# Performance work log

Measured on AMD Instinct MI355X. Metric: run time of the kernel, lower is better.

## Reference

```python
import jax, jax.numpy as jnp
import numpy as np

HQ, HKV, HD = 8, 4, 256          # query heads, kv heads, head dim
SW = 1024                         # sliding window (layer_idx=0 is even -> window active)
EPS = 1e-6
SCALE = 256.0 ** -0.5             # query_pre_attn_scalar ** -0.5
THETA = 10000.0
NEG = jnp.finfo(jnp.float32).min


def _rms_norm(x, w):
    # Gemma2 RMSNorm: fp32 variance, weight applied as (1 + kernel)
    var = jnp.mean(jnp.square(x.astype(jnp.float32)), axis=-1, keepdims=True)
    xn = x / jnp.sqrt(var + EPS)
    return (1.0 + w) * xn


def _rope(q, k, positions):
    # standard rotate-half RoPE over full head_dim
    inv = 1.0 / (THETA ** (jnp.arange(0, HD, 2, dtype=jnp.float32) / HD))  # [HD/2]
    freqs = positions.astype(jnp.float32)[..., None] * inv                  # [B,S,HD/2]
    emb = jnp.concatenate([freqs, freqs], axis=-1)                          # [B,S,HD]
    cos = jnp.cos(emb)[:, :, None, :]
    sin = jnp.sin(emb)[:, :, None, :]
    def rot(x):
        return jnp.concatenate([-x[..., HD // 2:], x[..., :HD // 2]], axis=-1)
    return q * cos + rot(q) * sin, k * cos + rot(k) * sin


def setup_inputs() -> dict:
    key = jax.random.key(0)
    ks = jax.random.split(key, 12)
    B, S, D, I = 1, 2048, 2304, 9216
    std = 0.02
    return {
        "hidden_states": jax.random.normal(ks[0], (B, S, D), jnp.float32),
        "attention_mask": jnp.ones((B, S), jnp.int32),
        "position_ids": jnp.broadcast_to(jnp.arange(S, dtype=jnp.int32)[None], (B, S)),
        "wq": jax.random.normal(ks[1], (D, HQ * HD), jnp.float32) * std,
        "wk": jax.random.normal(ks[2], (D, HKV * HD), jnp.float32) * std,
        "wv": jax.random.normal(ks[3], (D, HKV * HD), jnp.float32) * std,
        "wo": jax.random.normal(ks[4], (HQ * HD, D), jnp.float32) * std,
        "w_gate": jax.random.normal(ks[5], (D, I), jnp.float32) * std,
        "w_up": jax.random.normal(ks[6], (D, I), jnp.float32) * std,
        "w_down": jax.random.normal(ks[7], (I, D), jnp.float32) * std,
        "ln_in": jax.random.uniform(ks[8], (D,), jnp.float32) * 0.1,
        "ln_post_attn": jax.random.uniform(ks[9], (D,), jnp.float32) * 0.1,
        "ln_pre_ffn": jax.random.uniform(ks[10], (D,), jnp.float32) * 0.1,
        "ln_post_ffn": jax.random.uniform(ks[11], (D,), jnp.float32) * 0.1,
    }


def _attention(h, attention_mask, position_ids, wq, wk, wv, wo):
    B, S, _ = h.shape
    q = (h @ wq).reshape(B, S, HQ, HD)
    k = (h @ wk).reshape(B, S, HKV, HD)
    v = (h @ wv).reshape(B, S, HKV, HD)
    q, k = _rope(q, k, position_ids)
    # GQA: repeat kv heads
    groups = HQ // HKV
    k = jnp.repeat(k, groups, axis=2)  # [B,S,HQ,HD]
    v = jnp.repeat(v, groups, axis=2)
    # combined mask: causal AND within sliding window AND padding mask
    i = jnp.arange(S)[:, None]
    j = jnp.arange(S)[None, :]
    keep = (j <= i) & ((i - j) < SW)                       # [S,S]
    keep = keep[None, None] & (attention_mask[:, None, None, :] > 0)  # [B,1,S,S]
    bias = jnp.where(keep, 0.0, NEG).astype(jnp.float32)
    scores = jnp.einsum("bqhd,bkhd->bhqk", q, k) * SCALE + bias
    probs = jax.nn.softmax(scores, axis=-1)
    out = jnp.einsum("bhqk,bkhd->bqhd", probs, v).reshape(B, S, HQ * HD)
    return out @ wo


def reference(hidden_states, attention_mask, position_ids, wq, wk, wv, wo,
              w_gate, w_up, w_down, ln_in, ln_post_attn, ln_pre_ffn, ln_post_ffn):
    # Gemma2 decoder layer with sandwich norms
    residual = hidden_states
    h = _rms_norm(hidden_states, ln_in)
    attn = _attention(h, attention_mask, position_ids, wq, wk, wv, wo)
    h = _rms_norm(attn, ln_post_attn)
    x = residual + h
    residual = x
    h = _rms_norm(x, ln_pre_ffn)
    h = (jax.nn.gelu(h @ w_gate, approximate=True) * (h @ w_up)) @ w_down
    h = _rms_norm(h, ln_post_ffn)
    return residual + h
```

## Files before the change

kernel.cpp:

```cpp
#include <hip/hip_runtime.h>
#include <stdint.h>

typedef unsigned short u16;
typedef unsigned int u32;
typedef __bf16 bf16x8 __attribute__((ext_vector_type(8)));
typedef float f32x4 __attribute__((ext_vector_type(4)));

#define S_LEN 2048
#define DMODEL 2304
#define DFF 9216
#define NHQ 8
#define NHKV 4
#define HDIM 256
#define SWIN 1024

__device__ __forceinline__ u16 f2bf(float f) {
  u32 u = __float_as_uint(f);
  u = (u + 0x7FFFu + ((u >> 16) & 1)) >> 16;
  return (u16)u;
}
__device__ __forceinline__ float bf2f(u16 h) {
  return __uint_as_float(((u32)h) << 16);
}

__device__ __forceinline__ void gload_lds16(const void* g, void* l) {
  __builtin_amdgcn_global_load_lds((const __attribute__((address_space(1))) u32*)g,
                                   (__attribute__((address_space(3))) u32*)l, 16, 0, 0);
}

template <int N>
__device__ __forceinline__ void wait_vmcnt() {
  if constexpr (N == 0) asm volatile("s_waitcnt vmcnt(0)" ::: "memory");
  else if constexpr (N == 4) asm volatile("s_waitcnt vmcnt(4)" ::: "memory");
  else if constexpr (N == 5) asm volatile("s_waitcnt vmcnt(5)" ::: "memory");
  else if constexpr (N == 6) asm volatile("s_waitcnt vmcnt(6)" ::: "memory");
  else if constexpr (N == 8) asm volatile("s_waitcnt vmcnt(8)" ::: "memory");
}

__device__ __forceinline__ float gelu_t(float x) {
  float u = 0.7978845608f * (x + 0.044715f * x * x * x);
  float e = __expf(2.f * u);
  float t = 1.f - 2.f / (e + 1.f);
  return 0.5f * x * (1.f + t);
}

__global__ __launch_bounds__(256) void transpose_convert(
    const float* __restrict__ in, u16* __restrict__ out, int K, int N, int stride) {
  __shared__ float t[32][130];
  const int k0 = blockIdx.x * 32, n0 = blockIdx.y * 128;
  const int tx = threadIdx.x & 31, ty = threadIdx.x >> 5;
#pragma unroll
  for (int r = 0; r < 4; ++r) {
    const float4 v = *(const float4*)&in[(size_t)(k0 + ty + r * 8) * stride + n0 + 4 * tx];
    t[ty + r * 8][4 * tx + 0] = v.x;
    t[ty + r * 8][4 * tx + 1] = v.y;
    t[ty + r * 8][4 * tx + 2] = v.z;
    t[ty + r * 8][4 * tx + 3] = v.w;
  }
  __syncthreads();
  const int kk = threadIdx.x & 15, nn = threadIdx.x >> 4;
#pragma unroll
  for (int r = 0; r < 8; ++r) {
    const int n = nn + r * 16;
    const u32 p = (u32)f2bf(t[2 * kk][n]) | ((u32)f2bf(t[2 * kk + 1][n]) << 16);
    *(u32*)&out[(size_t)(n0 + n) * K + k0 + 2 * kk] = p;
  }
}

__global__ __launch_bounds__(256) void vpack_kernel(
    const float* __restrict__ qkvf, u16* __restrict__ vtile) {
  __shared__ float t[32][33];
  const int s0 = blockIdx.x * 32, d0 = blockIdx.y * 32, kvh = blockIdx.z;
  const int tx = threadIdx.x & 31, ty = threadIdx.x >> 5;
#pragma unroll
  for (int r = 0; r < 4; ++r)
    t[ty + r * 8][tx] = qkvf[(size_t)(s0 + ty + r * 8) * 4096 + 3072 + kvh * HDIM + d0 + tx];
  __syncthreads();
  const int kk = threadIdx.x & 15, nn = threadIdx.x >> 4;
#pragma unroll
  for (int r = 0; r < 2; ++r) {
    const int d = nn + r * 16;
    const u32 p = (u32)f2bf(t[2 * kk][d]) | ((u32)f2bf(t[2 * kk + 1][d]) << 16);
    *(u32*)&vtile[(((size_t)kvh * 64 + (s0 >> 5)) * 256 + d0 + d) * 32 + 2 * kk] = p;
  }
}

__device__ __forceinline__ float block_sumsq(const float* xr, int D) {
  float ss = 0.f;
  for (int d = threadIdx.x; d < D; d += 256) { float v = xr[d]; ss += v * v; }
#pragma unroll
  for (int m = 1; m < 64; m <<= 1) ss += __shfl_xor(ss, m, 64);
  __shared__ float red[4];
  if ((threadIdx.x & 63) == 0) red[threadIdx.x >> 6] = ss;
  __syncthreads();
  return red[0] + red[1] + red[2] + red[3];
}

__global__ __launch_bounds__(256) void rmsnorm_bf16_kernel(
    const float* __restrict__ x, const float* __restrict__ w, u16* __restrict__ o) {
  const int row = blockIdx.x;
  const float* xr = x + (size_t)row * DMODEL;
  float tot = block_sumsq(xr, DMODEL);
  float inv = rsqrtf(tot / DMODEL + 1e-6f);
  u16* orow = o + (size_t)row * DMODEL;
  for (int d = threadIdx.x; d < DMODEL; d += 256)
    orow[d] = f2bf((1.f + w[d]) * (xr[d] * inv));
}

__global__ __launch_bounds__(256) void rms_add_rms_kernel(
    const float* __restrict__ y0, const float* __restrict__ y1,
    const float* __restrict__ w1,
    const float* __restrict__ res, const float* __restrict__ w2,
    float* __restrict__ xres, u16* __restrict__ hn) {
  const int row = blockIdx.x;
  const float* yr0 = y0 + (size_t)row * DMODEL;
  const float* yr1 = y1 + (size_t)row * DMODEL;
  const float* rr = res + (size_t)row * DMODEL;
  __shared__ float red[2][4];
  float yv[9];
  float ss = 0.f;
#pragma unroll
  for (int e = 0; e < 9; ++e) {
    const int d = threadIdx.x + e * 256;
    yv[e] = yr0[d] + yr1[d];
    ss += yv[e] * yv[e];
  }
#pragma unroll
  for (int m = 1; m < 64; m <<= 1) ss += __shfl_xor(ss, m, 64);
  if ((threadIdx.x & 63) == 0) red[0][threadIdx.x >> 6] = ss;
  __syncthreads();
  const float inv1 = rsqrtf((red[0][0] + red[0][1] + red[0][2] + red[0][3]) / DMODEL + 1e-6f);
  float* xr = xres + (size_t)row * DMODEL;
  float xv[9];
  float ss2 = 0.f;
#pragma unroll
  for (int e = 0; e < 9; ++e) {
    const int d = threadIdx.x + e * 256;
    float x = rr[d] + (1.f + w1[d]) * (yv[e] * inv1);
    xv[e] = x;
    xr[d] = x;
    ss2 += x * x;
  }
#pragma unroll
  for (int m = 1; m < 64; m <<= 1) ss2 += __shfl_xor(ss2, m, 64);
  if ((threadIdx.x & 63) == 0) red[1][threadIdx.x >> 6] = ss2;
  __syncthreads();
  const float inv2 = rsqrtf((red[1][0] + red[1][1] + red[1][2] + red[1][3]) / DMODEL + 1e-6f);
  u16* hr = hn + (size_t)row * DMODEL;
#pragma unroll
  for (int e = 0; e < 9; ++e) {
    const int d = threadIdx.x + e * 256;
    hr[d] = f2bf((1.f + w2[d]) * (xv[e] * inv2));
  }
}

__global__ __launch_bounds__(256) void reduce8_rms_add_kernel(
    const u16* __restrict__ p, const float* __restrict__ w,
    const float* __restrict__ res, float* __restrict__ o) {
  const int row = blockIdx.x;
  const size_t PS = (size_t)S_LEN * DMODEL;
  const u16* pr = p + (size_t)row * DMODEL;
  float y[9];
  float ss = 0.f;
#pragma unroll
  for (int e = 0; e < 9; ++e) {
    const int d = threadIdx.x + e * 256;
    float v = 0.f;
#pragma unroll
    for (int k = 0; k < 8; ++k) v += bf2f(pr[d + k * PS]);
    y[e] = v;
    ss += v * v;
  }
#pragma unroll
  for (int m = 1; m < 64; m <<= 1) ss += __shfl_xor(ss, m, 64);
  __shared__ float red[4];
  if ((threadIdx.x & 63) == 0) red[threadIdx.x >> 6] = ss;
  __syncthreads();
  const float tot = red[0] + red[1] + red[2] + red[3];
  const float inv = rsqrtf(tot / DMODEL + 1e-6f);
  const float* rr = res + (size_t)row * DMODEL;
  float* orow = o + (size_t)row * DMODEL;
#pragma unroll
  for (int e = 0; e < 9; ++e) {
    const int d = threadIdx.x + e * 256;
    orow[d] = rr[d] + (1.f + w[d]) * (y[e] * inv);
  }
}

__global__ void rope_kernel(const float* __restrict__ qkv, const int* __restrict__ pos,
                            u16* __restrict__ qb, u16* __restrict__ kt) {
  const int s = blockIdx.x;
  const int t = threadIdx.x;
  float p = (float)pos[s];
  float inv = powf(10000.f, -(float)(2 * t) / (float)HDIM);
  float f = p * inv;
  float cs = cosf(f), sn = sinf(f);
  const float* row = qkv + (size_t)s * 4096;
  u16* qr = qb + (size_t)s * (NHQ * HDIM);
#pragma unroll
  for (int h = 0; h < NHQ; ++h) {
    float x1 = row[h * HDIM + t], x2 = row[h * HDIM + t + 128];
    qr[h * HDIM + t] = f2bf(x1 * cs - x2 * sn);
    qr[h * HDIM + t + 128] = f2bf(x2 * cs + x1 * sn);
  }
#pragma unroll
  for (int h = 0; h < NHKV; ++h) {
    u16* kr = kt + ((size_t)h * S_LEN + s) * HDIM;
    float x1 = row[2048 + h * HDIM + t], x2 = row[2048 + h * HDIM + t + 128];
    kr[t] = f2bf(x1 * cs - x2 * sn);
    kr[t + 128] = f2bf(x2 * cs + x1 * sn);
  }
}

template <int BN, int MODE, int BUFS>
__global__ __launch_bounds__(512) void gemm_pipe(
    const u16* __restrict__ A, const u16* __restrict__ Bt, const u16* __restrict__ Bt2,
    void* __restrict__ Cv, void* __restrict__ Cv2,
    int M, int N, int Klen, int LDK, int ntn, int n1,
    const u16* __restrict__ gptr) {
  constexpr bool DUAL = (MODE == 4);
  constexpr int CH_B = BN / 8;
  constexpr int CH_TOT = 16 + (DUAL ? 2 * CH_B : CH_B);
  constexpr int LPW = CH_TOT / 8;
  constexpr int TILE = CH_TOT * 512;
  constexpr int NFR = BN / 64;
  __shared__ __align__(16) u16 smem[BUFS * TILE];

  const int tid = threadIdx.x;
  const int lane = tid & 63, wave = tid >> 6;
  const int wr = wave >> 2, wc = wave & 3;
  const int l15 = lane & 15, l16 = lane >> 4;

  const int MB = M >> 7;
  const int nwg = gridDim.x;
  const int orig = blockIdx.x;
  const int q = nwg >> 3, r = nwg & 7, xcd = orig & 7, lidx = orig >> 3;
  const int wg = (xcd < r ? xcd * (q + 1) : r * (q + 1) + (xcd - r) * q) + lidx;
  const int tiles = MB * ntn;
  const int kz = wg / tiles, wgt = wg % tiles;
  const int bm = wgt % MB, bn = wgt / MB;
  const bool side2 = !DUAL && bn >= n1;
  const int bnl = side2 ? bn - n1 : bn;
  const u16* Bp = side2 ? Bt2 : Bt;

  const u16* Az = A + (size_t)kz * Klen;
  const u16* Bz = Bp + (size_t)kz * Klen;
  const int NT = Klen >> 6;

  const u16* src[LPW];
  const int swz = (((lane & 7) ^ (lane >> 3)) * 8);
#pragma unroll
  for (int i = 0; i < LPW; ++i) {
    const int c = wave * LPW + i;
    if (c < 16) src[i] = Az + (size_t)(bm * 128 + c * 8 + (lane >> 3)) * LDK + swz;
    else if (!DUAL || c < 16 + CH_B)
      src[i] = Bz + (size_t)(bnl * BN + (c - 16) * 8 + (lane >> 3)) * LDK + swz;
    else
      src[i] = Bt2 + (size_t)kz * Klen + (size_t)(bnl * BN + (c - 16 - CH_B) * 8 + (lane >> 3)) * LDK + swz;
  }
  const int dst0 = wave * LPW * 512 + lane * 8;

  auto STAGE = [&](int buf, int kt) {
    u16* base = smem + buf * TILE + dst0;
    const size_t ko = (size_t)kt * 64;
#pragma unroll
    for (int i = 0; i < LPW; ++i) gload_lds16(src[i] + ko, base + i * 512);
  };

  f32x4 acc[4][NFR];
  f32x4 acc2[DUAL ? 4 : 1][DUAL ? NFR : 1];
#pragma unroll
  for (int m = 0; m < 4; ++m)
#pragma unroll
    for (int n = 0; n < NFR; ++n) {
      acc[m][n] = f32x4{0.f, 0.f, 0.f, 0.f};
      if constexpr (DUAL) acc2[m][n] = f32x4{0.f, 0.f, 0.f, 0.f};
    }

  auto COMPUTE = [&](int buf) {
    const u16* Ab = smem + buf * TILE;
    const u16* Bb = Ab + 16 * 512;
    const u16* Ub = Ab + (16 + CH_B) * 512;
    bf16x8 a[2][4], b[2][NFR];
    bf16x8 u[DUAL ? 2 : 1][DUAL ? NFR : 1];
#pragma unroll
    for (int kk = 0; kk < 2; ++kk) {
      const int cc = kk * 4 + l16;
#pragma unroll
      for (int m = 0; m < 4; ++m) {
        const int rr = wr * 64 + m * 16 + l15;
        a[kk][m] = *(const bf16x8*)&Ab[rr * 64 + ((cc ^ (rr & 7)) * 8)];
      }
#pragma unroll
      for (int n = 0; n < NFR; ++n) {
        const int rr = wc * (BN / 4) + n * 16 + l15;
        b[kk][n] = *(const bf16x8*)&Bb[rr * 64 + ((cc ^ (rr & 7)) * 8)];
        if constexpr (DUAL)
          u[kk][n] = *(const bf16x8*)&Ub[rr * 64 + ((cc ^ (rr & 7)) * 8)];
      }
    }
    __builtin_amdgcn_s_setprio(1);
#pragma unroll
    for (int kk = 0; kk < 2; ++kk)
#pragma unroll
      for (int m = 0; m < 4; ++m)
#pragma unroll
        for (int n = 0; n < NFR; ++n)
          acc[m][n] = __builtin_amdgcn_mfma_f32_16x16x32_bf16(a[kk][m], b[kk][n], acc[m][n], 0, 0, 0);
    if constexpr (DUAL) {
#pragma unroll
      for (int kk = 0; kk < 2; ++kk)
#pragma unroll
        for (int m = 0; m < 4; ++m)
#pragma unroll
          for (int n = 0; n < NFR; ++n)
            acc2[m][n] = __builtin_amdgcn_mfma_f32_16x16x32_bf16(a[kk][m], u[kk][n], acc2[m][n], 0, 0, 0);
    }
    __builtin_amdgcn_s_setprio(0);
  };

  if constexpr (BUFS == 2) {
    STAGE(0, 0);
    wait_vmcnt<0>();
    __builtin_amdgcn_s_barrier();
    int cur = 0;
    for (int t = 0; t < NT; ++t) {
      if (t + 1 < NT) STAGE(cur ^ 1, t + 1);
      COMPUTE(cur);
      if (t + 1 < NT) { wait_vmcnt<0>(); __builtin_amdgcn_s_barrier(); }
      cur ^= 1;
    }
  } else {
    STAGE(0, 0);
    STAGE(1, 1);
    wait_vmcnt<LPW>();
    __builtin_amdgcn_s_barrier();
    int cur = 0;
    for (int t = 0; t < NT; ++t) {
      const int nb = (cur >= 1) ? cur - 1 : cur + 2;
      if (t + 2 < NT) STAGE(nb, t + 2);
      COMPUTE(cur);
      if (t + 1 < NT) {
        if (t + 2 < NT) wait_vmcnt<LPW>();
        else            wait_vmcnt<0>();
        __builtin_amdgcn_s_barrier();
      }
      cur = (cur == 2) ? 0 : cur + 1;
    }
  }

  const int row0 = bm * 128 + wr * 64 + l16 * 4;
  const int col0 = bnl * BN + wc * (BN / 4) + l15;
  float* Cf = (float*)(side2 ? Cv2 : Cv) + (size_t)kz * M * N;
  u16* Cb = (u16*)(side2 ? Cv2 : Cv) + (size_t)kz * M * N;
#pragma unroll
  for (int m = 0; m < 4; ++m)
#pragma unroll
    for (int n = 0; n < NFR; ++n)
#pragma unroll
      for (int rr = 0; rr < 4; ++rr) {
        const size_t idx = (size_t)(row0 + m * 16 + rr) * N + col0 + n * 16;
        if (MODE == 0) Cf[idx] = acc[m][n][rr];
        else if (MODE == 1) Cb[idx] = f2bf(acc[m][n][rr]);
        else if (MODE == 2) ((u16*)Cv)[idx] = f2bf(gelu_t(bf2f(gptr[idx])) * acc[m][n][rr]);
        else if (MODE == 4) {
          if constexpr (DUAL)
            ((u16*)Cv)[idx] = f2bf(gelu_t(acc[m][n][rr]) * acc2[m][n][rr]);
        }
      }
}

__global__ __launch_bounds__(256) void attn_kernel(
    const u16* __restrict__ qb, const u16* __restrict__ kt,
    const u16* __restrict__ vtile, const int* __restrict__ amask,
    u16* __restrict__ outp) {
  __shared__ __align__(16) u16 Ks[2][32 * 256];
  __shared__ __align__(16) u16 Vs[2][256 * 32];
  __shared__ __align__(16) u16 Ps[4][16 * 40];
  const int bid = blockIdx.x;
  const int qh = bid & 7;
  const int qblk = bid >> 3;
  const int kvh = qh >> 1;
  const int q0 = qblk * 64;
  const int tid = threadIdx.x, lane = tid & 63, wave = tid >> 6;
  const int qrow = q0 + wave * 16;
  const int l15 = lane & 15, l16 = lane >> 4;

  bf16x8 qf[8];
  {
    const u16* qp = qb + (size_t)(qrow + l15) * (NHQ * HDIM) + qh * HDIM + l16 * 8;
#pragma unroll
    for (int kc = 0; kc < 8; ++kc) qf[kc] = *(const bf16x8*)(qp + kc * 32);
  }
  f32x4 acc[16];
#pragma unroll
  for (int n = 0; n < 16; ++n) acc[n] = f32x4{0.f, 0.f, 0.f, 0.f};
  float mr[4] = {-1e30f, -1e30f, -1e30f, -1e30f};
  float sr[4] = {0.f, 0.f, 0.f, 0.f};

  int lo = q0 - (SWIN - 1); if (lo < 0) lo = 0; lo &= ~31;
  const int ntiles = ((q0 + 63 - lo) >> 5) + 1;

  const char* kbase = (const char*)(kt + (size_t)kvh * S_LEN * HDIM);
  const char* vbase = (const char*)(vtile + (size_t)kvh * 64 * 256 * 32);

  auto STAGEKV = [&](int buf, int key0) {
    const char* ksrc = kbase + (size_t)key0 * 512;
    const char* vsrc = vbase + (size_t)(key0 >> 5) * 16384;
#pragma unroll
    for (int i = 0; i < 4; ++i) {
      const int b = (wave * 4 + i) * 1024 + lane * 16;
      gload_lds16(ksrc + (b ^ (((b >> 9) & 7) << 4)), (char*)&Ks[buf][0] + (wave * 4 + i) * 1024);
    }
#pragma unroll
    for (int i = 0; i < 4; ++i) {
      const int b = (wave * 4 + i) * 1024 + lane * 16;
      gload_lds16(vsrc + (b ^ (((b >> 6) & 3) << 4)), (char*)&Vs[buf][0] + (wave * 4 + i) * 1024);
    }
  };

  STAGEKV(0, lo);
  wait_vmcnt<0>();
  __builtin_amdgcn_s_barrier();

  int cur = 0;
  for (int it = 0; it < ntiles; ++it) {
    const int key0 = lo + it * 32;
    const int am0 = amask[key0 + l15];
    const int am1 = amask[key0 + 16 + l15];
    if (it + 1 < ntiles) { STAGEKV(cur ^ 1, key0 + 32); wait_vmcnt<8>(); }
    else                 { wait_vmcnt<0>(); }
    __builtin_amdgcn_s_barrier();

    if (key0 <= qrow + 15 && key0 + 31 >= qrow - (SWIN - 1)) {
      f32x4 sc[2];
      sc[0] = f32x4{0.f, 0.f, 0.f, 0.f};
      sc[1] = f32x4{0.f, 0.f, 0.f, 0.f};
#pragma unroll
      for (int ct = 0; ct < 2; ++ct) {
        const int r = ct * 16 + l15;
#pragma unroll
        for (int kc = 0; kc < 8; ++kc) {
          const int byte = (r * 512 + kc * 64 + l16 * 16) ^ ((r & 7) << 4);
          bf16x8 kf = *(const bf16x8*)((const char*)&Ks[cur][0] + byte);
          sc[ct] = __builtin_amdgcn_mfma_f32_16x16x32_bf16(qf[kc], kf, sc[ct], 0, 0, 0);
        }
      }
      float pr[2][4];
#pragma unroll
      for (int ct = 0; ct < 2; ++ct) {
        const int j = key0 + ct * 16 + l15;
        const bool jok = (ct ? am1 : am0) > 0;
#pragma unroll
        for (int r = 0; r < 4; ++r) {
          const int i = qrow + l16 * 4 + r;
          const bool ok = jok && (j <= i) && (i - j < SWIN);
          pr[ct][r] = ok ? sc[ct][r] * 0.0625f : -1e30f;
        }
      }
      float resc[4];
#pragma unroll
      for (int r = 0; r < 4; ++r) {
        float mx = fmaxf(pr[0][r], pr[1][r]);
#pragma unroll
        for (int mm = 1; mm < 16; mm <<= 1) mx = fmaxf(mx, __shfl_xor(mx, mm, 64));
        const float mnew = fmaxf(mr[r], mx);
        const float rs = __expf(mr[r] - mnew);
        mr[r] = mnew;
        float p0 = __expf(pr[0][r] - mnew);
        float p1 = __expf(pr[1][r] - mnew);
        pr[0][r] = p0; pr[1][r] = p1;
        float sm = p0 + p1;
#pragma unroll
        for (int mm = 1; mm < 16; mm <<= 1) sm += __shfl_xor(sm, mm, 64);
        sr[r] = sr[r] * rs + sm;
        resc[r] = rs;
      }
#pragma unroll
      for (int n = 0; n < 16; ++n)
#pragma unroll
        for (int r = 0; r < 4; ++r) acc[n][r] *= resc[r];
      u16* P = &Ps[wave][0];
#pragma unroll
      for (int ct = 0; ct < 2; ++ct)
#pragma unroll
        for (int r = 0; r < 4; ++r)
          P[(l16 * 4 + r) * 40 + ct * 16 + l15] = f2bf(pr[ct][r]);
      bf16x8 pa = *(const bf16x8*)&P[l15 * 40 + l16 * 8];
#pragma unroll
      for (int n = 0; n < 16; ++n) {
        const int d = n * 16 + l15;
        const int byte = (d * 64 + l16 * 16) ^ ((d & 3) << 4);
        bf16x8 vf = *(const bf16x8*)((const char*)&Vs[cur][0] + byte);
        acc[n] = __builtin_amdgcn_mfma_f32_16x16x32_bf16(pa, vf, acc[n], 0, 0, 0);
      }
    }
    __builtin_amdgcn_s_barrier();
    cur ^= 1;
  }
#pragma unroll
  for (int n = 0; n < 16; ++n)
#pragma unroll
    for (int r = 0; r < 4; ++r) {
      const int i = qrow + l16 * 4 + r;
      outp[(size_t)i * (NHQ * HDIM) + qh * HDIM + n * 16 + l15] = f2bf(acc[n][r] / sr[r]);
    }
}

__global__ void gelu_mul_kernel(const u16* __restrict__ g, const u16* __restrict__ u,
                                u16* __restrict__ o, int n8) {
  const int idx0 = blockIdx.x * blockDim.x + threadIdx.x;
  const int stride = gridDim.x * blockDim.x;
  for (int i = idx0; i < n8; i += stride) {
    uint4 gv = ((const uint4*)g)[i];
    uint4 uv = ((const uint4*)u)[i];
    u32 gg[4] = {gv.x, gv.y, gv.z, gv.w};
    u32 uu[4] = {uv.x, uv.y, uv.z, uv.w};
    u32 ow[4];
#pragma unroll
    for (int w = 0; w < 4; ++w) {
      float x0 = bf2f((u16)(gg[w] & 0xffff)), x1 = bf2f((u16)(gg[w] >> 16));
      float y0 = bf2f((u16)(uu[w] & 0xffff)), y1 = bf2f((u16)(uu[w] >> 16));
      ow[w] = (u32)f2bf(gelu_t(x0) * y0) | ((u32)f2bf(gelu_t(x1) * y1) << 16);
    }
    ((uint4*)o)[i] = make_uint4(ow[0], ow[1], ow[2], ow[3]);
  }
}

extern "C" void kernel_launch(void* const* d_in, const int* in_sizes, int n_in,
                              void* d_out, int out_size, void* d_ws, size_t ws_size,
                              hipStream_t stream) {
  const float* hidden = (const float*)d_in[0];
  const int*   amask  = (const int*)d_in[1];
  const int*   pos    = (const int*)d_in[2];
  const float* wq     = (const float*)d_in[3];
  const float* wk     = (const float*)d_in[4];
  const float* wv     = (const float*)d_in[5];
  const float* wo     = (const float*)d_in[6];
  const float* wg     = (const float*)d_in[7];
  const float* wu     = (const float*)d_in[8];
  const float* wd     = (const float*)d_in[9];
  const float* ln_in  = (const float*)d_in[10];
  const float* ln_pa  = (const float*)d_in[11];
  const float* ln_pf  = (const float*)d_in[12];
  const float* ln_po  = (const float*)d_in[13];
  float* out = (float*)d_out;

  char* ws = (char*)d_ws;
  size_t off = 0;
  auto alloc = [&](size_t b) { char* p = ws + off; off += (b + 255) & ~(size_t)255; return p; };
  u16*   WT    = (u16*)alloc((size_t)DFF * DMODEL * 2);
  u16*   hnorm = (u16*)alloc((size_t)S_LEN * DMODEL * 2);
  char*  big0  = alloc((size_t)S_LEN * DFF * 2);
  u16*   qb    = (u16*)alloc((size_t)S_LEN * NHQ * HDIM * 2);
  u16*   ktb   = (u16*)alloc((size_t)NHKV * S_LEN * HDIM * 2);
  u16*   vtile = (u16*)alloc((size_t)NHKV * 64 * 256 * 32 * 2);
  u16*   attn  = (u16*)alloc((size_t)S_LEN * NHQ * HDIM * 2);
  float* f32t  = (float*)alloc((size_t)S_LEN * DMODEL * 4);
  float* xres  = (float*)alloc((size_t)S_LEN * DMODEL * 4);
  u16*   gbuf  = (u16*)alloc((size_t)S_LEN * DFF * 2);
  u16*   ubuf  = (u16*)alloc((size_t)S_LEN * DFF * 2);
  u16*   WTU   = (u16*)alloc((size_t)DFF * DMODEL * 2);
  const bool fused_gu = (off <= ws_size);
  (void)n_in; (void)in_sizes; (void)out_size; (void)f32t;
  float* qkvf = (float*)big0;
  u16*   ggu  = (u16*)big0;
  float* opart = (float*)big0;
  u16*   part = gbuf;
  const size_t PS = (size_t)S_LEN * DMODEL;

  const dim3 B256(256), B128(128), B512(512);

  rmsnorm_bf16_kernel<<<dim3(S_LEN), B256, 0, stream>>>(hidden, ln_in, hnorm);
  transpose_convert<<<dim3(DMODEL / 32, 2048 / 128), B256, 0, stream>>>(wq, WT, DMODEL, 2048, 2048);
  transpose_convert<<<dim3(DMODEL / 32, 1024 / 128), B256, 0, stream>>>(wk, WT + (size_t)2048 * DMODEL, DMODEL, 1024, 1024);
  transpose_convert<<<dim3(DMODEL / 32, 1024 / 128), B256, 0, stream>>>(wv, WT + (size_t)3072 * DMODEL, DMODEL, 1024, 1024);
  gemm_pipe<128, 0, 2><<<dim3(512), B512, 0, stream>>>(hnorm, WT, WT, qkvf, qkvf, S_LEN, 4096, DMODEL, DMODEL, 32, 32, nullptr);
  rope_kernel<<<dim3(S_LEN), B128, 0, stream>>>(qkvf, pos, qb, ktb);
  vpack_kernel<<<dim3(S_LEN / 32, HDIM / 32, NHKV), B256, 0, stream>>>(qkvf, vtile);
  attn_kernel<<<dim3((S_LEN / 64) * NHQ), B256, 0, stream>>>(qb, ktb, vtile, amask, attn);
  transpose_convert<<<dim3(2048 / 32, DMODEL / 128), B256, 0, stream>>>(wo, WT, 2048, DMODEL, DMODEL);
  gemm_pipe<192, 0, 2><<<dim3(384), B512, 0, stream>>>(attn, WT, WT, opart, opart, S_LEN, DMODEL, 1024, 2048, 12, 12, nullptr);
  rms_add_rms_kernel<<<dim3(S_LEN), B256, 0, stream>>>(opart, opart + PS, ln_pa, hidden, ln_pf, xres, hnorm);
  if (fused_gu) {
    transpose_convert<<<dim3(DMODEL / 32, DFF / 128), B256, 0, stream>>>(wg, WT, DMODEL, DFF, DFF);
    transpose_convert<<<dim3(DMODEL / 32, DFF / 128), B256, 0, stream>>>(wu, WTU, DMODEL, DFF, DFF);
    gemm_pipe<192, 4, 2><<<dim3(768), B512, 0, stream>>>(hnorm, WT, WTU, ggu, nullptr, S_LEN, DFF, DMODEL, DMODEL, 48, 48, nullptr);
  } else {
    transpose_convert<<<dim3(DMODEL / 32, DFF / 128), B256, 0, stream>>>(wg, WT, DMODEL, DFF, DFF);
    gemm_pipe<192, 1, 3><<<dim3(768), B512, 0, stream>>>(hnorm, WT, WT, gbuf, gbuf, S_LEN, DFF, DMODEL, DMODEL, 48, 48, nullptr);
    transpose_convert<<<dim3(DMODEL / 32, DFF / 128), B256, 0, stream>>>(wu, WT, DMODEL, DFF, DFF);
    gemm_pipe<192, 2, 3><<<dim3(768), B512, 0, stream>>>(hnorm, WT, WT, ggu, ggu, S_LEN, DFF, DMODEL, DMODEL, 48, 48, gbuf);
  }
  transpose_convert<<<dim3(DFF / 32, DMODEL / 128), B256, 0, stream>>>(wd, WT, DFF, DMODEL, DMODEL);
  gemm_pipe<192, 1, 2><<<dim3(1536), B512, 0, stream>>>(ggu, WT, WT, part, part, S_LEN, DMODEL, DFF / 8, DFF, 12, 12, nullptr);
  reduce8_rms_add_kernel<<<dim3(S_LEN), B256, 0, stream>>>(part, ln_po, xres, out);
}
```

Measured before the change: 575.6 us.

## Prefetch next tile's LDS fragments during MFMA in triple-buffered GEMM; retile fused gate/up

Splits the GEMM compute step into per-k LDS fragment reads and MFMA batches. In the 3-buffer path it reads the next tile's first k-slice while the current tile's second MFMA batch runs, so LDS latency is hidden behind matrix math. It also waits for all outstanding loads each iteration. Separately, the fused gate/up GEMM switches from BN=192 with 2 buffers to BN=128 with 3 buffers and a larger grid. The cost is more register pressure from fragments held across the barrier, plus more blocks with smaller tiles.

```diff
diff --git a/kernel.cpp b/kernel.cpp
--- a/kernel.cpp
+++ b/kernel.cpp
@@ -1,5 +1,6 @@
 #include <hip/hip_runtime.h>
 #include <stdint.h>
+#include <type_traits>
 
 typedef unsigned short u16;
 typedef unsigned int u32;
@@ -13,6 +14,8 @@
 #define NHKV 4
 #define HDIM 256
 #define SWIN 1024
+
+template <int N> using IC = std::integral_constant<int, N>;
 
 __device__ __forceinline__ u16 f2bf(float f) {
   u32 u = __float_as_uint(f);
@@ -277,44 +280,43 @@
       if constexpr (DUAL) acc2[m][n] = f32x4{0.f, 0.f, 0.f, 0.f};
     }
 
-  auto COMPUTE = [&](int buf) {
+  bf16x8 a[2][4], b[2][NFR];
+  bf16x8 u[DUAL ? 2 : 1][DUAL ? NFR : 1];
+
+  auto READK = [&](auto kkc, int buf) {
+    constexpr int kk = decltype(kkc)::value;
     const u16* Ab = smem + buf * TILE;
     const u16* Bb = Ab + 16 * 512;
     const u16* Ub = Ab + (16 + CH_B) * 512;
-    bf16x8 a[2][4], b[2][NFR];
-    bf16x8 u[DUAL ? 2 : 1][DUAL ? NFR : 1];
-#pragma unroll
-    for (int kk = 0; kk < 2; ++kk) {
-      const int cc = kk * 4 + l16;
-#pragma unroll
-      for (int m = 0; m < 4; ++m) {
-        const int rr = wr * 64 + m * 16 + l15;
-        a[kk][m] = *(const bf16x8*)&Ab[rr * 64 + ((cc ^ (rr & 7)) * 8)];
-      }
-#pragma unroll
-      for (int n = 0; n < NFR; ++n) {
-        const int rr = wc * (BN / 4) + n * 16 + l15;
-        b[kk][n] = *(const bf16x8*)&Bb[rr * 64 + ((cc ^ (rr & 7)) * 8)];
-        if constexpr (DUAL)
-          u[kk][n] = *(const bf16x8*)&Ub[rr * 64 + ((cc ^ (rr & 7)) * 8)];
-      }
-    }
+    const int cc = kk * 4 + l16;
+#pragma unroll
+    for (int m = 0; m < 4; ++m) {
+      const int rr = wr * 64 + m * 16 + l15;
+      a[kk][m] = *(const bf16x8*)&Ab[rr * 64 + ((cc ^ (rr & 7)) * 8)];
+    }
+#pragma unroll
+    for (int n = 0; n < NFR; ++n) {
+      const int rr = wc * (BN / 4) + n * 16 + l15;
+      b[kk][n] = *(const bf16x8*)&Bb[rr * 64 + ((cc ^ (rr & 7)) * 8)];
+      if constexpr (DUAL)
+        u[kk][n] = *(const bf16x8*)&Ub[rr * 64 + ((cc ^ (rr & 7)) * 8)];
+    }
+  };
+
+  auto MFMAK = [&](auto kkc) {
+    constexpr int kk = decltype(kkc)::value;
     __builtin_amdgcn_s_setprio(1);
 #pragma unroll
-    for (int kk = 0; kk < 2; ++kk)
+    for (int m = 0; m < 4; ++m)
+#pragma unroll
+      for (int n = 0; n < NFR; ++n)
+        acc[m][n] = __builtin_amdgcn_mfma_f32_16x16x32_bf16(a[kk][m], b[kk][n], acc[m][n], 0, 0, 0);
+    if constexpr (DUAL) {
 #pragma unroll
       for (int m = 0; m < 4; ++m)
 #pragma unroll
         for (int n = 0; n < NFR; ++n)
-          acc[m][n] = __builtin_amdgcn_mfma_f32_16x16x32_bf16(a[kk][m], b[kk][n], acc[m][n], 0, 0, 0);
-    if constexpr (DUAL) {
-#pragma unroll
-      for (int kk = 0; kk < 2; ++kk)
-#pragma unroll
-        for (int m = 0; m < 4; ++m)
-#pragma unroll
-          for (int n = 0; n < NFR; ++n)
-            acc2[m][n] = __builtin_amdgcn_mfma_f32_16x16x32_bf16(a[kk][m], u[kk][n], acc2[m][n], 0, 0, 0);
+          acc2[m][n] = __builtin_amdgcn_mfma_f32_16x16x32_bf16(a[kk][m], u[kk][n], acc2[m][n], 0, 0, 0);
     }
     __builtin_amdgcn_s_setprio(0);
   };
@@ -326,26 +328,30 @@
     int cur = 0;
     for (int t = 0; t < NT; ++t) {
       if (t + 1 < NT) STAGE(cur ^ 1, t + 1);
-      COMPUTE(cur);
+      READK(IC<0>{}, cur);
+      READK(IC<1>{}, cur);
+      MFMAK(IC<0>{});
+      MFMAK(IC<1>{});
       if (t + 1 < NT) { wait_vmcnt<0>(); __builtin_amdgcn_s_barrier(); }
       cur ^= 1;
     }
   } else {
     STAGE(0, 0);
     STAGE(1, 1);
-    wait_vmcnt<LPW>();
+    wait_vmcnt<0>();
     __builtin_amdgcn_s_barrier();
+    READK(IC<0>{}, 0);
     int cur = 0;
     for (int t = 0; t < NT; ++t) {
-      const int nb = (cur >= 1) ? cur - 1 : cur + 2;
-      if (t + 2 < NT) STAGE(nb, t + 2);
-      COMPUTE(cur);
-      if (t + 1 < NT) {
-        if (t + 2 < NT) wait_vmcnt<LPW>();
-        else            wait_vmcnt<0>();
-        __builtin_amdgcn_s_barrier();
-      }
-      cur = (cur == 2) ? 0 : cur + 1;
+      const int nxt = (cur == 2) ? 0 : cur + 1;
+      const int fre = (nxt == 2) ? 0 : nxt + 1;
+      if (t + 2 < NT) STAGE(fre, t + 2);
+      READK(IC<1>{}, cur);
+      MFMAK(IC<0>{});
+      if (t + 1 < NT) READK(IC<0>{}, nxt);
+      MFMAK(IC<1>{});
+      if (t + 1 < NT) { wait_vmcnt<0>(); __builtin_amdgcn_s_barrier(); }
+      cur = nxt;
     }
   }
 
@@ -585,7 +591,7 @@
   if (fused_gu) {
     transpose_convert<<<dim3(DMODEL / 32, DFF / 128), B256, 0, stream>>>(wg, WT, DMODEL, DFF, DFF);
     transpose_convert<<<dim3(DMODEL / 32, DFF / 128), B256, 0, stream>>>(wu, WTU, DMODEL, DFF, DFF);
-    gemm_pipe<192, 4, 2><<<dim3(768), B512, 0, stream>>>(hnorm, WT, WTU, ggu, nullptr, S_LEN, DFF, DMODEL, DMODEL, 48, 48, nullptr);
+    gemm_pipe<128, 4, 3><<<dim3(1152), B512, 0, stream>>>(hnorm, WT, WTU, ggu, nullptr, S_LEN, DFF, DMODEL, DMODEL, 72, 72, nullptr);
   } else {
     transpose_convert<<<dim3(DMODEL / 32, DFF / 128), B256, 0, stream>>>(wg, WT, DMODEL, DFF, DFF);
     gemm_pipe<192, 1, 3><<<dim3(768), B512, 0, stream>>>(hnorm, WT, WT, gbuf, gbuf, S_LEN, DFF, DMODEL, DMODEL, 48, 48, nullptr);
```

Result: slower. 643.9 us (+11.9%).
